# Performance work log

Measured on AMD Instinct MI355X. Metric: run time of the kernel, lower is better.

The kernel has to match this reference:

```python
import jax, jax.numpy as jnp
import numpy as np

T, B = 512, 128
F_IN = 32 * 32 + 6   # encoded_classes*encoded_categories + action_features = 1030
H = 512              # hidden_state_size


def setup_inputs() -> dict:
    key = jax.random.key(0)
    k1, k2, k3, k4, k5 = jax.random.split(key, 5)
    s_i = 1.0 / np.sqrt(F_IN)
    s_h = 1.0 / np.sqrt(H)
    return {
        "hidden_state": jnp.zeros((B, H), jnp.float32),            # initial carry (module uses zeros)
        "gru_input": jax.random.normal(k1, (T, B, F_IN), jnp.float32),  # time-major [T,B,F]
        # fused input-projection weights for gates (r, z, n): [F, 3H] + bias [3H]
        "Wi": jax.random.uniform(k2, (F_IN, 3 * H), jnp.float32, -s_i, s_i),
        "bi": jnp.zeros((3 * H,), jnp.float32),
        # hidden projections: r,z have no bias in flax GRUCell; n has its own bias
        "Wh_rz": jax.random.uniform(k3, (H, 2 * H), jnp.float32, -s_h, s_h),
        "Wh_n": jax.random.uniform(k4, (H, H), jnp.float32, -s_h, s_h),
        "bh_n": jnp.zeros((H,), jnp.float32),
    }


def reference(hidden_state, gru_input, Wi, bi, Wh_rz, Wh_n, bh_n):
    # flax GRUCell with gate_fn=silu, activation_fn=tanh:
    #   r = silu(x@Wir + bir + h@Whr)
    #   z = silu(x@Wiz + biz + h@Whz)
    #   h' = (1-z)*n + z*h
    # Precompute all input projections in one big GEMM: [T,B,3H]
    xg = jnp.einsum("tbf,fg->tbg", gru_input, Wi) + bi

    def step(h, x):
        xr, xz, xn = jnp.split(x, 3, axis=-1)
        hr, hz = jnp.split(h @ Wh_rz, 2, axis=-1)
        r = jax.nn.silu(xr + hr)
        z = jax.nn.silu(xz + hz)
        n = jnp.tanh(xn + r * (h @ Wh_n + bh_n))
        h_new = (1.0 - z) * n + z * h
        return h_new, h_new

    carry, ys = jax.lax.scan(step, hidden_state, xg)
    # nnx.RNN(return_carry=True, time_major=True) -> (final_carry [B,H], outputs [T,B,H])
    return carry, ys
```

## Files before the change

kernel.cpp:

```cpp
#include <hip/hip_runtime.h>
#include <cstddef>
#include <cstdint>


#define T_STEPS 512
#define BATCH   128
#define F_IN    1030
#define KPAD    1056
#define H       512
#define G3      1536
#define TCHUNK  32
#define NCHUNK  (T_STEPS / TCHUNK)
#define MCHUNK  (TCHUNK * BATCH)
#define NTILE_M (MCHUNK / 128)
#define NTILE_N (G3 / 256)
#define NTILE   (NTILE_M * NTILE_N)
#define RBLK    128
#define NWORK   120
#define FPAGE   4096
#define BUFU32  32768

using f32x4  = __attribute__((ext_vector_type(4)))  float;
using bf16x8 = __attribute__((ext_vector_type(8)))  short;
using u16x8  = __attribute__((ext_vector_type(8)))  unsigned short;
using u32x4  = __attribute__((ext_vector_type(4)))  unsigned int;

__device__ __forceinline__ unsigned short f2bf(float f) {
    unsigned int u = __builtin_bit_cast(unsigned int, f);
    u = (u + 0x7FFFu + ((u >> 16) & 1u)) >> 16;
    return (unsigned short)u;
}
__device__ __forceinline__ float bf2f(unsigned short s) {
    unsigned int u = ((unsigned int)s) << 16;
    return __builtin_bit_cast(float, u);
}
__device__ __forceinline__ unsigned int cvt2bf(float lo, float hi) {
    unsigned int r;
    asm("v_cvt_pk_bf16_f32 %0, %1, %2" : "=v"(r) : "v"(lo), "v"(hi));
    return r;
}
__device__ __forceinline__ void ld4_coh(const unsigned int* p, u32x4& d) {
    asm volatile("global_load_dwordx4 %0, %1, off sc0 sc1"
                 : "=&v"(d) : "v"(p) : "memory");
}

__global__ __launch_bounds__(256) void transpose_wi(const float* __restrict__ Wi,
                                                    unsigned short* __restrict__ wiT) {
    __shared__ float t_lds[32][33];
    const int kx = blockIdx.x, gy = blockIdx.y;
    const int tx = threadIdx.x, ty = threadIdx.y;
#pragma unroll
    for (int r = 0; r < 4; ++r) {
        int k = kx * 32 + ty + r * 8;
        int g = gy * 32 + tx;
        t_lds[ty + r * 8][tx] = (k < F_IN) ? Wi[(size_t)k * G3 + g] : 0.f;
    }
    __syncthreads();
#pragma unroll
    for (int r = 0; r < 4; ++r) {
        int g = gy * 32 + ty + r * 8;
        int k = kx * 32 + tx;
        wiT[(size_t)g * KPAD + k] = f2bf(t_lds[tx][ty + r * 8]);
    }
}

__global__ __launch_bounds__(256) void transpose_wh(const float* __restrict__ Whrz,
                                                    const float* __restrict__ Whn,
                                                    unsigned short* __restrict__ whT) {
    __shared__ float t_lds[32][33];
    const int kx = blockIdx.x, cy = blockIdx.y;
    const int tx = threadIdx.x, ty = threadIdx.y;
#pragma unroll
    for (int r = 0; r < 4; ++r) {
        int k = kx * 32 + ty + r * 8;
        int c = cy * 32 + tx;
        float v = (c < 1024) ? Whrz[(size_t)k * 1024 + c]
                             : Whn[(size_t)k * H + (c - 1024)];
        t_lds[ty + r * 8][tx] = v;
    }
    __syncthreads();
#pragma unroll
    for (int r = 0; r < 4; ++r) {
        int c = cy * 32 + ty + r * 8;
        int k = kx * 32 + tx;
        whT[(size_t)c * H + k] = f2bf(t_lds[tx][ty + r * 8]);
    }
}

__global__ __launch_bounds__(256) void init_ws(const float* __restrict__ h0,
                                               unsigned short* __restrict__ hx,
                                               unsigned int* __restrict__ flags) {
    int i = blockIdx.x * 256 + threadIdx.x;
    flags[i] = 0u;
    if (i < BATCH * H) hx[i] = f2bf(h0[i]);
}

__global__ __launch_bounds__(256) void gemm_xg(const float* __restrict__ x,
                                               const unsigned short* __restrict__ wiT,
                                               const float* __restrict__ bi,
                                               unsigned short* __restrict__ xg) {
    __shared__ unsigned short a_lds[128][40];
    __shared__ unsigned short b_lds[128][40];
    const int tid = threadIdx.x;
    const int n0 = blockIdx.x * 128;
    const int m0 = blockIdx.y * 128;
    const int l = tid & 63, w = tid >> 6;
    const int wr = w >> 1, wc = w & 1;
    const int sr = tid >> 1;
    const int sk = (tid & 1) * 16;

    f32x4 acc[4][4] = {};

    for (int kt = 0; kt < 33; ++kt) {
        if (kt) __syncthreads();
        {
            const int kb = kt * 32 + sk;
            const float* srcp = x + (size_t)(m0 + sr) * F_IN + kb;
            float2 f2v[8];
#pragma unroll
            for (int i = 0; i < 8; ++i) {
                int k = kb + 2 * i;
                if (k < F_IN) f2v[i] = *(const float2*)(srcp + 2 * i);
                else          f2v[i] = make_float2(0.f, 0.f);
            }
            uint4 p0, p1;
            p0.x = cvt2bf(f2v[0].x, f2v[0].y); p0.y = cvt2bf(f2v[1].x, f2v[1].y);
            p0.z = cvt2bf(f2v[2].x, f2v[2].y); p0.w = cvt2bf(f2v[3].x, f2v[3].y);
            p1.x = cvt2bf(f2v[4].x, f2v[4].y); p1.y = cvt2bf(f2v[5].x, f2v[5].y);
            p1.z = cvt2bf(f2v[6].x, f2v[6].y); p1.w = cvt2bf(f2v[7].x, f2v[7].y);
            *(uint4*)&a_lds[sr][sk]     = p0;
            *(uint4*)&a_lds[sr][sk + 8] = p1;
            const unsigned short* bsrc = wiT + (size_t)(n0 + sr) * KPAD + kb;
            *(uint4*)&b_lds[sr][sk]     = *(const uint4*)bsrc;
            *(uint4*)&b_lds[sr][sk + 8] = *(const uint4*)(bsrc + 8);
        }
        __syncthreads();
        const int ka = (l >> 4) * 8;
        bf16x8 af[4], bfr[4];
#pragma unroll
        for (int mi = 0; mi < 4; ++mi)
            af[mi] = *(const bf16x8*)&a_lds[wr * 64 + mi * 16 + (l & 15)][ka];
#pragma unroll
        for (int nj = 0; nj < 4; ++nj)
            bfr[nj] = *(const bf16x8*)&b_lds[wc * 64 + nj * 16 + (l & 15)][ka];
#pragma unroll
        for (int mi = 0; mi < 4; ++mi)
#pragma unroll
            for (int nj = 0; nj < 4; ++nj)
                acc[mi][nj] = __builtin_amdgcn_mfma_f32_16x16x32_bf16(
                    af[mi], bfr[nj], acc[mi][nj], 0, 0, 0);
    }

#pragma unroll
    for (int nj = 0; nj < 4; ++nj) {
        const int col = n0 + wc * 64 + nj * 16 + (l & 15);
        const float bv = bi[col];
#pragma unroll
        for (int mi = 0; mi < 4; ++mi) {
#pragma unroll
            for (int q = 0; q < 4; ++q) {
                const int row = m0 + wr * 64 + mi * 16 + (l >> 4) * 4 + q;
                xg[(size_t)row * G3 + col] = f2bf(acc[mi][nj][q] + bv);
            }
        }
    }
}

__global__ __launch_bounds__(512) void fused_chunk(
    const float* __restrict__ x_next,
    const unsigned short* __restrict__ wiT,
    const float* __restrict__ bi,
    unsigned short* __restrict__ xg_next,
    const unsigned short* __restrict__ xg_cur,
    const unsigned short* __restrict__ whT,
    const float* __restrict__ bhn,
    const float* __restrict__ hinit,
    unsigned short* __restrict__ hx,
    float* __restrict__ ys,
    float* __restrict__ carry,
    unsigned int* __restrict__ fpage,
    int t0, int do_gemm)
{
    __shared__ __align__(16) unsigned char smem[83200];
    const int tid = threadIdx.x;
    const int bid = blockIdx.x;
    const int l = tid & 63, w = tid >> 6;

    if (bid >= RBLK) {
        if (!do_gemm) return;
        unsigned short (*a_lds)[40] = (unsigned short(*)[40])smem;
        unsigned short (*b_lds)[40] = (unsigned short(*)[40])(smem + 10240);
        const int wr = w & 1, wc = w >> 1;
        const int sa_r = tid >> 2;
        const int sa_k = (tid & 3) * 8;
        const int sb_r = tid >> 1;
        const int sb_k = (tid & 1) * 16;

        for (int tile = bid - RBLK; tile < NTILE; tile += NWORK) {
            const int m0 = (tile & (NTILE_M - 1)) * 128;
            const int n0 = (tile / NTILE_M) * 256;
            f32x4 acc[4][4] = {};
            for (int kt = 0; kt < 33; ++kt) {
                __syncthreads();
                {
                    const int kb = kt * 32 + sa_k;
                    const float* srcp = x_next + (size_t)(m0 + sa_r) * F_IN + kb;
                    float2 f2v[4];
#pragma unroll
                    for (int i = 0; i < 4; ++i) {
                        int k = kb + 2 * i;
                        if (k < F_IN) f2v[i] = *(const float2*)(srcp + 2 * i);
                        else          f2v[i] = make_float2(0.f, 0.f);
                    }
                    uint4 p;
                    p.x = cvt2bf(f2v[0].x, f2v[0].y); p.y = cvt2bf(f2v[1].x, f2v[1].y);
                    p.z = cvt2bf(f2v[2].x, f2v[2].y); p.w = cvt2bf(f2v[3].x, f2v[3].y);
                    *(uint4*)&a_lds[sa_r][sa_k] = p;
                    const int kbB = kt * 32 + sb_k;
                    const unsigned short* bsrc = wiT + (size_t)(n0 + sb_r) * KPAD + kbB;
                    *(uint4*)&b_lds[sb_r][sb_k]     = *(const uint4*)bsrc;
                    *(uint4*)&b_lds[sb_r][sb_k + 8] = *(const uint4*)(bsrc + 8);
                }
                __syncthreads();
                const int ka = (l >> 4) * 8;
                bf16x8 af[4], bfr[4];
#pragma unroll
                for (int mi = 0; mi < 4; ++mi)
                    af[mi] = *(const bf16x8*)&a_lds[wr * 64 + mi * 16 + (l & 15)][ka];
#pragma unroll
                for (int nj = 0; nj < 4; ++nj)
                    bfr[nj] = *(const bf16x8*)&b_lds[wc * 64 + nj * 16 + (l & 15)][ka];
#pragma unroll
                for (int mi = 0; mi < 4; ++mi)
#pragma unroll
                    for (int nj = 0; nj < 4; ++nj)
                        acc[mi][nj] = __builtin_amdgcn_mfma_f32_16x16x32_bf16(
                            af[mi], bfr[nj], acc[mi][nj], 0, 0, 0);
            }
#pragma unroll
            for (int nj = 0; nj < 4; ++nj) {
                const int col = n0 + wc * 64 + nj * 16 + (l & 15);
                const float bv = bi[col];
#pragma unroll
                for (int mi = 0; mi < 4; ++mi) {
#pragma unroll
                    for (int q = 0; q < 4; ++q) {
                        const int row = m0 + wr * 64 + mi * 16 + (l >> 4) * 4 + q;
                        xg_next[(size_t)row * G3 + col] = f2bf(acc[mi][nj][q] + bv);
                    }
                }
            }
            __syncthreads();
        }
        return;
    }

    unsigned short (*wlds)[16][520] = (unsigned short(*)[16][520])smem;
    unsigned short (*h_lds)[520]    = (unsigned short(*)[520])(smem + 49920);
    unsigned int* hl32 = (unsigned int*)(smem + 49920);

    const int grp = bid >> 5;
    const int rnk = bid & 31;
    const int b0 = grp * 32;
    const int j0 = rnk * 16;
    unsigned int* flbase = fpage + grp * 1024;
    unsigned int* flown  = flbase + rnk * 32;
    const unsigned int* hx32 = (const unsigned int*)hx;
    unsigned int* hx32w = (unsigned int*)hx;

#pragma unroll
    for (int it = 0; it < 6; ++it) {
        int L = tid + it * 512;
        int gate = L >> 10;
        int rem = L & 1023;
        int jj = rem >> 6;
        int k8 = (rem & 63) * 8;
        *(u16x8*)&wlds[gate][jj][k8] =
            *(const u16x8*)(whT + ((size_t)(gate * H + j0 + jj)) * H + k8);
    }

    const int col = j0 + (l & 15);
    float hreg[4];
    if (w < 2) {
#pragma unroll
        for (int q = 0; q < 4; ++q) {
            const int row = w * 16 + (l >> 4) * 4 + q;
            hreg[q] = hinit[(size_t)(b0 + row) * H + col];
        }
    }
    const float bnv = bhn[col];
    const int hrow = tid >> 4;
    const int hseg = tid & 15;

    for (int s = 0; s < TCHUNK; ++s) {
        const int t = t0 + s;
        unsigned short pxr[4], pxz[4], pxn[4];
        if (w < 2) {
#pragma unroll
            for (int q = 0; q < 4; ++q) {
                const int row = w * 16 + (l >> 4) * 4 + q;
                const size_t rb = ((size_t)s * BATCH + b0 + row) * G3;
                pxr[q] = xg_cur[rb + col];
                pxz[q] = xg_cur[rb + H + col];
                pxn[q] = xg_cur[rb + 2 * H + col];
            }
        }
        if (s > 0) {
            if (w == 0) {
                int guard = 0;
                for (;;) {
                    unsigned int fv = 0xFFFFFFFFu;
                    if (l < 32)
                        fv = __hip_atomic_load(flbase + l * 32, __ATOMIC_RELAXED,
                                               __HIP_MEMORY_SCOPE_AGENT);
                    if (__all((int)(fv >= (unsigned int)s))) break;
                    if (++guard > 4096) break;
                    __builtin_amdgcn_s_sleep(1);
                }
            }
            __syncthreads();
        }
        const unsigned int* hsrc = hx32 + (size_t)(t & 1) * BUFU32
                                 + grp * 8192 + hrow * 256 + hseg * 16;
        u32x4 hv0, hv1, hv2, hv3;
        ld4_coh(hsrc + 0,  hv0);
        ld4_coh(hsrc + 4,  hv1);
        ld4_coh(hsrc + 8,  hv2);
        ld4_coh(hsrc + 12, hv3);
        asm volatile("s_waitcnt vmcnt(0)" ::: "memory");
        {
            unsigned int* d = &hl32[hrow * 260 + hseg * 16];
            *(u32x4*)(d + 0)  = hv0;
            *(u32x4*)(d + 4)  = hv1;
            *(u32x4*)(d + 8)  = hv2;
            *(u32x4*)(d + 12) = hv3;
        }
        __syncthreads();
        if (w < 2) {
            f32x4 a0 = {}, a1 = {}, a2 = {};
#pragma unroll
            for (int kt = 0; kt < 16; ++kt) {
                const int ko = kt * 32 + (l >> 4) * 8;
                bf16x8 a = *(const bf16x8*)&h_lds[w * 16 + (l & 15)][ko];
                bf16x8 b0v = *(const bf16x8*)&wlds[0][l & 15][ko];
                bf16x8 b1v = *(const bf16x8*)&wlds[1][l & 15][ko];
                bf16x8 b2v = *(const bf16x8*)&wlds[2][l & 15][ko];
                a0 = __builtin_amdgcn_mfma_f32_16x16x32_bf16(a, b0v, a0, 0, 0, 0);
                a1 = __builtin_amdgcn_mfma_f32_16x16x32_bf16(a, b1v, a1, 0, 0, 0);
                a2 = __builtin_amdgcn_mfma_f32_16x16x32_bf16(a, b2v, a2, 0, 0, 0);
            }
            float* yst = ys + (size_t)t * BATCH * H;
            unsigned int* hdst = hx32w + (size_t)((t + 1) & 1) * BUFU32 + grp * 8192;
            unsigned short hb[4];
#pragma unroll
            for (int q = 0; q < 4; ++q) {
                const float pr = bf2f(pxr[q]) + a0[q];
                const float pz = bf2f(pxz[q]) + a1[q];
                const float r = pr / (1.f + __expf(-pr));
                const float z = pz / (1.f + __expf(-pz));
                const float n = tanhf(bf2f(pxn[q]) + r * (a2[q] + bnv));
                const float ho = (1.f - z) * n + z * hreg[q];
                hreg[q] = ho;
                hb[q] = f2bf(ho);
                const int row = w * 16 + (l >> 4) * 4 + q;
                const size_t o = (size_t)(b0 + row) * H + col;
                yst[o] = ho;
                if (t == T_STEPS - 1) carry[o] = ho;
            }
#pragma unroll
            for (int q = 0; q < 4; ++q) {
                unsigned int other = __shfl_xor((unsigned int)hb[q], 1);
                if ((l & 1) == 0) {
                    const int row = w * 16 + (l >> 4) * 4 + q;
                    unsigned int val = (unsigned int)hb[q] | (other << 16);
                    __hip_atomic_store(hdst + row * 256 + (col >> 1), val,
                                       __ATOMIC_RELAXED, __HIP_MEMORY_SCOPE_AGENT);
                }
            }
        }
        __syncthreads();
        if (tid == 0)
            __hip_atomic_store(flown, (unsigned int)(s + 1),
                               __ATOMIC_RELAXED, __HIP_MEMORY_SCOPE_AGENT);
    }
}

extern "C" void kernel_launch(void* const* d_in, const int* in_sizes, int n_in,
                              void* d_out, int out_size, void* d_ws, size_t ws_size,
                              hipStream_t stream) {
    const float* h0   = (const float*)d_in[0];
    const float* x    = (const float*)d_in[1];
    const float* Wi   = (const float*)d_in[2];
    const float* bi   = (const float*)d_in[3];
    const float* Whrz = (const float*)d_in[4];
    const float* Whn  = (const float*)d_in[5];
    const float* bhn  = (const float*)d_in[6];

    float* carry = (float*)d_out;
    float* ys    = (float*)d_out + (size_t)BATCH * H;

    unsigned short* wiT  = (unsigned short*)d_ws;
    unsigned short* whT  = wiT + (size_t)G3 * KPAD;
    unsigned short* xgb0 = whT + (size_t)G3 * H;
    unsigned short* xgb1 = xgb0 + (size_t)MCHUNK * G3;
    unsigned short* hx   = xgb1 + (size_t)MCHUNK * G3;
    unsigned int*   flags = (unsigned int*)(hx + (size_t)2 * BATCH * H);

    transpose_wi<<<dim3(KPAD / 32, G3 / 32), dim3(32, 8), 0, stream>>>(Wi, wiT);
    transpose_wh<<<dim3(H / 32, G3 / 32), dim3(32, 8), 0, stream>>>(Whrz, Whn, whT);
    init_ws<<<dim3(256), 256, 0, stream>>>(h0, hx, flags);

    gemm_xg<<<dim3(G3 / 128, MCHUNK / 128), 256, 0, stream>>>(x, wiT, bi, xgb0);

    for (int c = 0; c < NCHUNK; ++c) {
        const int t0 = c * TCHUNK;
        unsigned short* xg_cur  = (c & 1) ? xgb1 : xgb0;
        unsigned short* xg_next = (c & 1) ? xgb0 : xgb1;
        const float* hinit = (c == 0) ? h0 : ys + (size_t)(t0 - 1) * BATCH * H;
        const float* x_next = (c + 1 < NCHUNK) ? x + (size_t)(c + 1) * MCHUNK * F_IN
                                               : x;
        fused_chunk<<<dim3(RBLK + NWORK), 512, 0, stream>>>(
            x_next, wiT, bi, xg_next, xg_cur, whT, bhn, hinit,
            hx, ys, carry, flags + (size_t)c * FPAGE, t0,
            (c + 1 < NCHUNK) ? 1 : 0);
    }
}
```

Measured before the change: 2.044 ms.

## Publish per-wave step flags early and poll peers with a dedicated wave

Each compute wave now writes its own progress flag right after its h stores drain, before writing ys and carry, so peer blocks can start sooner. Polling moves to a spare wave (w==7) that runs during the MFMA compute, and the next step's h load and xg prefetch are merged into one post-barrier phase. This cuts one barrier per step and shortens the critical path of the cross-block recurrence. The risk is more flag traffic, since 64 flags per group are polled instead of 32.

```diff
diff --git a/kernel.cpp b/kernel.cpp
--- a/kernel.cpp
+++ b/kernel.cpp
@@ -264,7 +264,7 @@
     const int b0 = grp * 32;
     const int j0 = rnk * 16;
     unsigned int* flbase = fpage + grp * 1024;
-    unsigned int* flown  = flbase + rnk * 32;
+    unsigned int* flown  = flbase + (rnk * 2 + w) * 16;
     const unsigned int* hx32 = (const unsigned int*)hx;
     unsigned int* hx32w = (unsigned int*)hx;
 
@@ -292,35 +292,8 @@
     const int hrow = tid >> 4;
     const int hseg = tid & 15;
 
-    for (int s = 0; s < TCHUNK; ++s) {
-        const int t = t0 + s;
-        unsigned short pxr[4], pxz[4], pxn[4];
-        if (w < 2) {
-#pragma unroll
-            for (int q = 0; q < 4; ++q) {
-                const int row = w * 16 + (l >> 4) * 4 + q;
-                const size_t rb = ((size_t)s * BATCH + b0 + row) * G3;
-                pxr[q] = xg_cur[rb + col];
-                pxz[q] = xg_cur[rb + H + col];
-                pxn[q] = xg_cur[rb + 2 * H + col];
-            }
-        }
-        if (s > 0) {
-            if (w == 0) {
-                int guard = 0;
-                for (;;) {
-                    unsigned int fv = 0xFFFFFFFFu;
-                    if (l < 32)
-                        fv = __hip_atomic_load(flbase + l * 32, __ATOMIC_RELAXED,
-                                               __HIP_MEMORY_SCOPE_AGENT);
-                    if (__all((int)(fv >= (unsigned int)s))) break;
-                    if (++guard > 4096) break;
-                    __builtin_amdgcn_s_sleep(1);
-                }
-            }
-            __syncthreads();
-        }
-        const unsigned int* hsrc = hx32 + (size_t)(t & 1) * BUFU32
+    {
+        const unsigned int* hsrc = hx32 + (size_t)(t0 & 1) * BUFU32
                                  + grp * 8192 + hrow * 256 + hseg * 16;
         u32x4 hv0, hv1, hv2, hv3;
         ld4_coh(hsrc + 0,  hv0);
@@ -328,14 +301,27 @@
         ld4_coh(hsrc + 8,  hv2);
         ld4_coh(hsrc + 12, hv3);
         asm volatile("s_waitcnt vmcnt(0)" ::: "memory");
-        {
-            unsigned int* d = &hl32[hrow * 260 + hseg * 16];
-            *(u32x4*)(d + 0)  = hv0;
-            *(u32x4*)(d + 4)  = hv1;
-            *(u32x4*)(d + 8)  = hv2;
-            *(u32x4*)(d + 12) = hv3;
-        }
-        __syncthreads();
+        unsigned int* d = &hl32[hrow * 260 + hseg * 16];
+        *(u32x4*)(d + 0)  = hv0;
+        *(u32x4*)(d + 4)  = hv1;
+        *(u32x4*)(d + 8)  = hv2;
+        *(u32x4*)(d + 12) = hv3;
+    }
+    unsigned short pxr[4], pxz[4], pxn[4];
+    if (w < 2) {
+#pragma unroll
+        for (int q = 0; q < 4; ++q) {
+            const int row = w * 16 + (l >> 4) * 4 + q;
+            const size_t rb = ((size_t)(b0 + row)) * G3;
+            pxr[q] = xg_cur[rb + col];
+            pxz[q] = xg_cur[rb + H + col];
+            pxn[q] = xg_cur[rb + 2 * H + col];
+        }
+    }
+    __syncthreads();
+
+    for (int s = 0; s < TCHUNK; ++s) {
+        const int t = t0 + s;
         if (w < 2) {
             f32x4 a0 = {}, a1 = {}, a2 = {};
 #pragma unroll
@@ -349,9 +335,9 @@
                 a1 = __builtin_amdgcn_mfma_f32_16x16x32_bf16(a, b1v, a1, 0, 0, 0);
                 a2 = __builtin_amdgcn_mfma_f32_16x16x32_bf16(a, b2v, a2, 0, 0, 0);
             }
-            float* yst = ys + (size_t)t * BATCH * H;
             unsigned int* hdst = hx32w + (size_t)((t + 1) & 1) * BUFU32 + grp * 8192;
             unsigned short hb[4];
+            float ho4[4];
 #pragma unroll
             for (int q = 0; q < 4; ++q) {
                 const float pr = bf2f(pxr[q]) + a0[q];
@@ -361,11 +347,8 @@
                 const float n = tanhf(bf2f(pxn[q]) + r * (a2[q] + bnv));
                 const float ho = (1.f - z) * n + z * hreg[q];
                 hreg[q] = ho;
+                ho4[q] = ho;
                 hb[q] = f2bf(ho);
-                const int row = w * 16 + (l >> 4) * 4 + q;
-                const size_t o = (size_t)(b0 + row) * H + col;
-                yst[o] = ho;
-                if (t == T_STEPS - 1) carry[o] = ho;
             }
 #pragma unroll
             for (int q = 0; q < 4; ++q) {
@@ -377,11 +360,57 @@
                                        __ATOMIC_RELAXED, __HIP_MEMORY_SCOPE_AGENT);
                 }
             }
+            asm volatile("s_waitcnt vmcnt(0)" ::: "memory");
+            if (l == 0)
+                __hip_atomic_store(flown, (unsigned int)(s + 1),
+                                   __ATOMIC_RELAXED, __HIP_MEMORY_SCOPE_AGENT);
+            float* yst = ys + (size_t)t * BATCH * H;
+#pragma unroll
+            for (int q = 0; q < 4; ++q) {
+                const int row = w * 16 + (l >> 4) * 4 + q;
+                const size_t o = (size_t)(b0 + row) * H + col;
+                yst[o] = ho4[q];
+                if (t == T_STEPS - 1) carry[o] = ho4[q];
+            }
+        } else if (w == 7 && s + 1 < TCHUNK) {
+            const unsigned int tgt = (unsigned int)(s + 1);
+            int guard = 0;
+            for (;;) {
+                unsigned int fv = __hip_atomic_load(flbase + l * 16,
+                                                    __ATOMIC_RELAXED,
+                                                    __HIP_MEMORY_SCOPE_AGENT);
+                if (__all((int)(fv >= tgt))) break;
+                if (++guard > 8192) break;
+                __builtin_amdgcn_s_sleep(1);
+            }
         }
         __syncthreads();
-        if (tid == 0)
-            __hip_atomic_store(flown, (unsigned int)(s + 1),
-                               __ATOMIC_RELAXED, __HIP_MEMORY_SCOPE_AGENT);
+        if (s + 1 < TCHUNK) {
+            const unsigned int* hsrc = hx32 + (size_t)((t + 1) & 1) * BUFU32
+                                     + grp * 8192 + hrow * 256 + hseg * 16;
+            u32x4 hv0, hv1, hv2, hv3;
+            ld4_coh(hsrc + 0,  hv0);
+            ld4_coh(hsrc + 4,  hv1);
+            ld4_coh(hsrc + 8,  hv2);
+            ld4_coh(hsrc + 12, hv3);
+            if (w < 2) {
+#pragma unroll
+                for (int q = 0; q < 4; ++q) {
+                    const int row = w * 16 + (l >> 4) * 4 + q;
+                    const size_t rb = ((size_t)(s + 1) * BATCH + b0 + row) * G3;
+                    pxr[q] = xg_cur[rb + col];
+                    pxz[q] = xg_cur[rb + H + col];
+                    pxn[q] = xg_cur[rb + 2 * H + col];
+                }
+            }
+            asm volatile("s_waitcnt vmcnt(0)" ::: "memory");
+            unsigned int* d = &hl32[hrow * 260 + hseg * 16];
+            *(u32x4*)(d + 0)  = hv0;
+            *(u32x4*)(d + 4)  = hv1;
+            *(u32x4*)(d + 8)  = hv2;
+            *(u32x4*)(d + 12) = hv3;
+            __syncthreads();
+        }
     }
 }
 
```

Measured after the change: 2.421 ms. +18.5%, slower.
